# Optimization experiments

Hardware: AMD Instinct MI355X
Metric: run time of the kernel (lower is better)

The kernel has to match this reference:

```python
import jax, jax.numpy as jnp
import numpy as np

N = 100000   # nodes per graph (protein == ligand node count, forced by cat dim=1)
E = 3200000  # edges per graph (avg degree 32)
F = 128      # input feature dim
A = 10       # action dim


def _fanin_uniform(key, shape, fanin=None):
    fanin = fanin or shape[0]
    v = 1.0 / np.sqrt(fanin)
    return jax.random.uniform(key, shape, jnp.float32, -v, v)


def setup_inputs() -> dict:
    key = jax.random.key(0)
    ks = jax.random.split(key, 24)
    inp = {
        "protein_x": jax.random.normal(ks[0], (N, F), jnp.float32),
        "protein_edges": jax.random.randint(ks[1], (2, E), 0, N, jnp.int32),
        "ligand_x": jax.random.normal(ks[2], (N, F), jnp.float32),
        "ligand_edges": jax.random.randint(ks[3], (2, E), 0, N, jnp.int32),
        "action": jax.random.normal(ks[4], (N, A), jnp.float32),
        # protein GraphConv layers
        "wp1s": _fanin_uniform(ks[5], (F, 16)),
        "wp1n": _fanin_uniform(ks[6], (F, 16)),
        "bp1": jnp.zeros((16,), jnp.float32),
        "wp2s": _fanin_uniform(ks[7], (16, 50)),
        "wp2n": _fanin_uniform(ks[8], (16, 50)),
        "bp2": jnp.zeros((50,), jnp.float32),
        # ligand GraphConv layers
        "wl1s": _fanin_uniform(ks[9], (F, 16)),
        "wl1n": _fanin_uniform(ks[10], (F, 16)),
        "bl1": jnp.zeros((16,), jnp.float32),
        "wl2s": _fanin_uniform(ks[11], (16, 50)),
        "wl2n": _fanin_uniform(ks[12], (16, 50)),
        "bl2": jnp.zeros((50,), jnp.float32),
        # MLP head
        "w_in": _fanin_uniform(ks[13], (100, 60)),
        "b_in": jnp.zeros((60,), jnp.float32),
        "w_hid": _fanin_uniform(ks[14], (60 + A, 10)),
        "b_hid": jnp.zeros((10,), jnp.float32),
        "w_out": jax.random.uniform(ks[15], (10, 1), jnp.float32, -0.003, 0.003),
        "b_out": jnp.zeros((1,), jnp.float32),
    }
    return inp


def graph_conv(x, edge_index, w_self, w_nbr, b):
    # PyG GraphConv: x_i' = x_i @ W_self + (sum_{j->i} x_j) @ W_nbr + b
    src, dst = edge_index[0], edge_index[1]
    agg = jax.ops.segment_sum(x[src], dst, num_segments=x.shape[0])  # [N, Fin]
    return x @ w_self + agg @ w_nbr + b


def reference(protein_x, protein_edges, ligand_x, ligand_edges, action,
              wp1s, wp1n, bp1, wp2s, wp2n, bp2,
              wl1s, wl1n, bl1, wl2s, wl2n, bl2,
              w_in, b_in, w_hid, b_hid, w_out, b_out):
    # protein branch (dropout is identity in eval mode)
    p = jax.nn.relu(graph_conv(protein_x, protein_edges, wp1s, wp1n, bp1))
    p = graph_conv(p, protein_edges, wp2s, wp2n, bp2)            # [N, 50]
    # ligand branch
    l = jax.nn.relu(graph_conv(ligand_x, ligand_edges, wl1s, wl1n, bl1))
    l = graph_conv(l, ligand_edges, wl2s, wl2n, bl2)             # [N, 50]
    molecule = jnp.concatenate([p, l], axis=1)                   # [N, 100]
    finger_print = jax.nn.relu(molecule @ w_in + b_in)           # [N, 60]
    policy = jnp.concatenate([finger_print, action], axis=1) @ w_hid + b_hid
    policy = jax.nn.relu(policy) @ w_out + b_out                 # [N, 1]
    return policy
```

## Files before the change

### kernel.cpp

```cpp
#include <hip/hip_runtime.h>
#include <hip/hip_bf16.h>
#include <stdint.h>


#define F_IN 128
#define NBMAX 512
#define BIN_CH 16
#define BIN_EDGES (256 * BIN_CH)
#define FINE_CAP 12288

#define OW1P  0
#define OB1P  4096
#define OW1L  4112
#define OB1L  8208
#define OC1P  8224
#define OC2P  9184
#define OC1L  10144
#define OC2L  11104
#define OBIN  12064
#define OWHID 12124
#define OBHID 12824
#define OWOUT 12834
#define OBOUT 12844
#define WBUF_FLOATS 16384

__device__ __forceinline__ float bf2f(unsigned short u) {
    union { unsigned int i; float f; } v; v.i = ((unsigned int)u) << 16; return v.f;
}
__device__ __forceinline__ float bflo(unsigned int u) {
    union { unsigned int i; float f; } v; v.i = u << 16; return v.f;
}
__device__ __forceinline__ float bfhi(unsigned int u) {
    union { unsigned int i; float f; } v; v.i = u & 0xffff0000u; return v.f;
}
__device__ __forceinline__ unsigned short f2bf(float f) {
    union { float f; unsigned int i; } v; v.f = f;
    unsigned int u = v.i;
    unsigned int r = (u + 0x7fffu + ((u >> 16) & 1u)) >> 16;
    return (unsigned short)r;
}
__device__ __forceinline__ unsigned pack2bf(float a, float b) {
    return (unsigned)f2bf(a) | ((unsigned)f2bf(b) << 16);
}
__device__ __forceinline__ float ldf(const void* p, int isf32, size_t i) {
    return isf32 ? ((const float*)p)[i] : bf2f(((const unsigned short*)p)[i]);
}


struct PW {
    const void *wp1s, *wp1n, *bp1, *wl1s, *wl1n, *bl1;
    const void *wp2s, *wp2n, *bp2, *wl2s, *wl2n, *bl2;
    const void *w_in, *b_in, *w_hid, *b_hid, *w_out, *b_out;
};

__global__ __launch_bounds__(256) void k_prepw(
    PW P, const unsigned short* __restrict__ px, float* __restrict__ wb,
    int* __restrict__ flag, int* __restrict__ zp, int zn)
{
    __shared__ int cnt_s;
    if (threadIdx.x == 0) cnt_s = 0;
    __syncthreads();
    int bad = 0;
    for (int i = threadIdx.x; i < 4096; i += 256) {
        unsigned e = (px[i] >> 7) & 0xFFu;
        if (e >= 140u) bad++;
    }
    atomicAdd(&cnt_s, bad);
    __syncthreads();
    const int isf32 = (cnt_s > 4096 / 16) ? 1 : 0;
    if (threadIdx.x == 0 && blockIdx.x == 0) *flag = isf32;

    int t = blockIdx.x * 256 + threadIdx.x;
    int stride = gridDim.x * 256;
    for (int i = t; i < zn; i += stride) zp[i] = 0;

    for (int i = t; i < 4096; i += stride) {
        int k = i >> 5, j = i & 31;
        wb[OW1P + i] = (j < 16) ? ldf(P.wp1s, isf32, k * 16 + j)
                                : ldf(P.wp1n, isf32, k * 16 + (j - 16));
        wb[OW1L + i] = (j < 16) ? ldf(P.wl1s, isf32, k * 16 + j)
                                : ldf(P.wl1n, isf32, k * 16 + (j - 16));
    }
    for (int i = t; i < 16; i += stride) {
        wb[OB1P + i] = ldf(P.bp1, isf32, i);
        wb[OB1L + i] = ldf(P.bl1, isf32, i);
    }
    for (int i = t; i < 960; i += stride) {
        int k = i / 60, j = i % 60;
        float s1 = 0.f, s2 = 0.f;
        for (int r = 0; r < 50; ++r) {
            float wi = ldf(P.w_in, isf32, r * 60 + j);
            s1 += ldf(P.wp2s, isf32, k * 50 + r) * wi;
            s2 += ldf(P.wp2n, isf32, k * 50 + r) * wi;
        }
        wb[OC1P + i] = s1; wb[OC2P + i] = s2;
    }
    for (int i = t; i < 960; i += stride) {
        int k = i / 60, j = i % 60;
        float s1 = 0.f, s2 = 0.f;
        for (int r = 0; r < 50; ++r) {
            float wi = ldf(P.w_in, isf32, (50 + r) * 60 + j);
            s1 += ldf(P.wl2s, isf32, k * 50 + r) * wi;
            s2 += ldf(P.wl2n, isf32, k * 50 + r) * wi;
        }
        wb[OC1L + i] = s1; wb[OC2L + i] = s2;
    }
    for (int i = t; i < 60; i += stride) {
        float s = ldf(P.b_in, isf32, i);
        for (int r = 0; r < 50; ++r) {
            s += ldf(P.bp2, isf32, r) * ldf(P.w_in, isf32, r * 60 + i);
            s += ldf(P.bl2, isf32, r) * ldf(P.w_in, isf32, (50 + r) * 60 + i);
        }
        wb[OBIN + i] = s;
    }
    for (int i = t; i < 700; i += stride) wb[OWHID + i] = ldf(P.w_hid, isf32, i);
    for (int i = t; i < 10; i += stride) {
        wb[OBHID + i] = ldf(P.b_hid, isf32, i);
        wb[OWOUT + i] = ldf(P.w_out, isf32, i);
    }
    if (t == 0) wb[OBOUT] = ldf(P.b_out, isf32, 0);
}


__global__ __launch_bounds__(256) void k_bucket_hist(
    const int* __restrict__ ed0, const int* __restrict__ ed1,
    int* __restrict__ cnt, int nE)
{
    const int* ed = blockIdx.y ? ed1 : ed0;
    int* c = cnt + blockIdx.y * NBMAX;
    __shared__ int h[NBMAX];
    for (int i = threadIdx.x; i < NBMAX; i += 256) h[i] = 0;
    __syncthreads();
    int gid = blockIdx.x * 256 + threadIdx.x;
    int stride = gridDim.x * 256;
    int nE4 = nE >> 2;
    const int4* ed4 = (const int4*)ed;
    for (int i = gid; i < nE4; i += stride) {
        int4 v = ed4[i];
        atomicAdd(&h[v.x >> 8], 1);
        atomicAdd(&h[v.y >> 8], 1);
        atomicAdd(&h[v.z >> 8], 1);
        atomicAdd(&h[v.w >> 8], 1);
    }
    for (int e = (nE4 << 2) + gid; e < nE; e += stride)
        atomicAdd(&h[ed[e] >> 8], 1);
    __syncthreads();
    for (int i = threadIdx.x; i < NBMAX; i += 256)
        if (h[i]) atomicAdd(&c[i], h[i]);
}

__global__ __launch_bounds__(512) void k_bucket_scan(
    const int* __restrict__ cnt, int* __restrict__ base,
    int* __restrict__ cursor, int nb)
{
    const int* c = cnt + blockIdx.x * NBMAX;
    int* ba = base + blockIdx.x * 528;
    int* cu = cursor + blockIdx.x * NBMAX;
    __shared__ int sh[512];
    int t = threadIdx.x;
    int v = (t < nb) ? c[t] : 0;
    sh[t] = v;
    __syncthreads();
    for (int off = 1; off < 512; off <<= 1) {
        int x = (t >= off) ? sh[t - off] : 0;
        __syncthreads();
        sh[t] += x;
        __syncthreads();
    }
    int excl = sh[t] - v;
    if (t < nb) { ba[t] = excl; cu[t] = excl; }
    if (t == nb - 1) ba[nb] = excl + v;
}

__global__ __launch_bounds__(256) void k_bucket_bin(
    const int* __restrict__ es0, const int* __restrict__ ed0,
    const int* __restrict__ es1, const int* __restrict__ ed1,
    int* __restrict__ cursor, unsigned* __restrict__ pairs, int nE)
{
    const int* es = blockIdx.y ? es1 : es0;
    const int* ed = blockIdx.y ? ed1 : ed0;
    int* cur = cursor + blockIdx.y * NBMAX;
    unsigned* pr = pairs + (size_t)blockIdx.y * nE;

    __shared__ int h[NBMAX];
    __shared__ int lcur[NBMAX];
    __shared__ int sh[256];
    __shared__ unsigned stage[BIN_EDGES];
    __shared__ unsigned short stageB[BIN_EDGES];

    for (int i = threadIdx.x; i < NBMAX; i += 256) h[i] = 0;
    __syncthreads();
    int e0 = blockIdx.x * BIN_EDGES;
    int eb = e0 + threadIdx.x * BIN_CH;
    int s[BIN_CH], d[BIN_CH];
    if (eb + BIN_CH <= nE) {
#pragma unroll
        for (int k4 = 0; k4 < BIN_CH / 4; ++k4) {
            int4 sv = *(const int4*)(es + eb + k4 * 4);
            int4 dv = *(const int4*)(ed + eb + k4 * 4);
            s[k4 * 4 + 0] = sv.x; d[k4 * 4 + 0] = dv.x;
            s[k4 * 4 + 1] = sv.y; d[k4 * 4 + 1] = dv.y;
            s[k4 * 4 + 2] = sv.z; d[k4 * 4 + 2] = dv.z;
            s[k4 * 4 + 3] = sv.w; d[k4 * 4 + 3] = dv.w;
        }
#pragma unroll
        for (int k = 0; k < BIN_CH; ++k)
            atomicAdd(&h[d[k] >> 8], 1);
    } else {
#pragma unroll
        for (int k = 0; k < BIN_CH; ++k) {
            int e = eb + k;
            if (e < nE) {
                s[k] = es[e]; d[k] = ed[e];
                atomicAdd(&h[d[k] >> 8], 1);
            } else d[k] = -1;
        }
    }
    __syncthreads();
    {
        int t = threadIdx.x;
        int a = h[2 * t], b2 = h[2 * t + 1];
        sh[t] = a + b2;
        __syncthreads();
        for (int off = 1; off < 256; off <<= 1) {
            int x = (t >= off) ? sh[t - off] : 0;
            __syncthreads();
            sh[t] += x;
            __syncthreads();
        }
        int excl = sh[t] - (a + b2);
        lcur[2 * t] = excl;
        lcur[2 * t + 1] = excl + a;
    }
    __syncthreads();
    for (int b = threadIdx.x; b < NBMAX; b += 256) {
        int c = h[b];
        if (c) {
            int g = atomicAdd(&cur[b], c);
            h[b] = g - lcur[b];
        }
    }
    __syncthreads();
    if (eb + BIN_CH <= nE) {
#pragma unroll
        for (int k = 0; k < BIN_CH; ++k) {
            int b = d[k] >> 8;
            int pos = atomicAdd(&lcur[b], 1);
            stage[pos] = ((unsigned)(d[k] & 255) << 24) | (unsigned)s[k];
            stageB[pos] = (unsigned short)b;
        }
    } else {
#pragma unroll
        for (int k = 0; k < BIN_CH; ++k) {
            if (d[k] >= 0) {
                int b = d[k] >> 8;
                int pos = atomicAdd(&lcur[b], 1);
                stage[pos] = ((unsigned)(d[k] & 255) << 24) | (unsigned)s[k];
                stageB[pos] = (unsigned short)b;
            }
        }
    }
    __syncthreads();
    int total = nE - e0; if (total > BIN_EDGES) total = BIN_EDGES;
    for (int i = threadIdx.x; i < total; i += 256)
        pr[h[stageB[i]] + i] = stage[i];
}

__global__ __launch_bounds__(512) void k_bucket_fine(
    const unsigned* __restrict__ pairs, const int* __restrict__ base,
    int* __restrict__ row0, int* __restrict__ srcs0,
    int* __restrict__ row1, int* __restrict__ srcs1,
    int n, int nE, int nb)
{
    const unsigned* pr = pairs + (size_t)blockIdx.y * nE;
    const int* ba = base + blockIdx.y * 528;
    int* row = blockIdx.y ? row1 : row0;
    int* srcs = blockIdx.y ? srcs1 : srcs0;
    __shared__ int cnt[256], cur[256];
    __shared__ int stage[FINE_CAP];
    int b = blockIdx.x;
    int t = threadIdx.x;
    int s0 = ba[b], s1 = ba[b + 1];
    int m = s1 - s0;
    if (t < 256) cnt[t] = 0;
    __syncthreads();
    for (int i = s0 + t; i < s1; i += 512)
        atomicAdd(&cnt[pr[i] >> 24], 1);
    __syncthreads();
    int c = (t < 256) ? cnt[t] : 0;
    if (t < 256) cur[t] = c;
    __syncthreads();
    for (int off = 1; off < 256; off <<= 1) {
        int x = (t < 256 && t >= off) ? cur[t - off] : 0;
        __syncthreads();
        if (t < 256) cur[t] += x;
        __syncthreads();
    }
    int excl = (t < 256) ? (cur[t] - c) : 0;
    __syncthreads();
    int node = (b << 8) + t;
    if (t < 256 && node < n) row[node] = s0 + excl;
    if (b == nb - 1 && t == 0) row[n] = nE;
    if (m <= FINE_CAP) {
        if (t < 256) cur[t] = excl;
        __syncthreads();
        for (int i = s0 + t; i < s1; i += 512) {
            unsigned p = pr[i];
            int slot = atomicAdd(&cur[p >> 24], 1);
            stage[slot] = (int)(p & 0xFFFFFFu);
        }
        __syncthreads();
        for (int i = t; i < m; i += 512)
            srcs[s0 + i] = stage[i];
    } else {
        if (t < 256) cur[t] = s0 + excl;
        __syncthreads();
        for (int i = s0 + t; i < s1; i += 512) {
            unsigned p = pr[i];
            int slot = atomicAdd(&cur[p >> 24], 1);
            srcs[slot] = (int)(p & 0xFFFFFFu);
        }
    }
}


struct TArgs2 {
    const void* __restrict__ x;
    const float* __restrict__ w;
    const float* __restrict__ b;
    float* __restrict__ acc;
    void* __restrict__ nbr;
};

__global__ __launch_bounds__(512) void k_transform1(
    TArgs2 a0, TArgs2 a1, int n, const int* __restrict__ flag)
{
    TArgs2 A = blockIdx.y ? a1 : a0;
    const int isf32 = *flag;
    __shared__ float xs[64 * 128];
    const int t = threadIdx.x;
    const int tile0 = blockIdx.x * 64;

    if (isf32) {
        const float4* xg = (const float4*)A.x;
        float4* xl = (float4*)xs;
#pragma unroll
        for (int i = 0; i < 4; ++i) {
            int flat = i * 512 + t;
            int row = flat >> 5, ck = flat & 31;
            if (tile0 + row < n)
                xl[row * 32 + (ck ^ (row & 7))] =
                    xg[((size_t)(tile0 + row)) * 32 + ck];
        }
    } else {
        const uint4* xg = (const uint4*)A.x;
        float4* xl = (float4*)xs;
#pragma unroll
        for (int i = 0; i < 2; ++i) {
            int flat = i * 512 + t;
            int row = flat >> 4, ck = flat & 15;
            if (tile0 + row < n) {
                uint4 q = xg[((size_t)(tile0 + row)) * 16 + ck];
                float4 lo = make_float4(bflo(q.x), bfhi(q.x), bflo(q.y), bfhi(q.y));
                float4 hi = make_float4(bflo(q.z), bfhi(q.z), bflo(q.w), bfhi(q.w));
                xl[row * 32 + ((2 * ck) ^ (row & 7))] = lo;
                xl[row * 32 + ((2 * ck + 1) ^ (row & 7))] = hi;
            }
        }
    }
    __syncthreads();

    const int jq = __builtin_amdgcn_readfirstlane(t >> 6);
    const int r = t & 63;
    const int node = tile0 + r;
    if (node >= n) return;
    const float* __restrict__ Wb = A.w + 4 * jq;
    const int sw = r & 7;

    float acc[4];
    if (jq < 4) {
#pragma unroll
        for (int j = 0; j < 4; ++j) acc[j] = A.b[4 * jq + j];
    } else {
#pragma unroll
        for (int j = 0; j < 4; ++j) acc[j] = 0.f;
    }

    const float4* xl = (const float4*)xs + r * 32;
    for (int kb = 0; kb < 4; ++kb) {
        float4 xq[8];
#pragma unroll
        for (int u = 0; u < 8; ++u)
            xq[u] = xl[(kb * 8 + u) ^ sw];
#pragma unroll
        for (int u = 0; u < 8; ++u) {
            int kk = kb * 8 + u;
            float xv[4] = {xq[u].x, xq[u].y, xq[u].z, xq[u].w};
#pragma unroll
            for (int h = 0; h < 4; ++h) {
                const float* __restrict__ w0 = Wb + (kk * 4 + h) * 32;
#pragma unroll
                for (int j = 0; j < 4; ++j) acc[j] += xv[h] * w0[j];
            }
        }
    }

    if (jq < 4) {
        float4* a4 = (float4*)(A.acc + (size_t)node * 16);
        a4[jq] = make_float4(acc[0], acc[1], acc[2], acc[3]);
    } else {
        unsigned short* nrow = (unsigned short*)A.nbr + ((size_t)node << 4)
                               + ((jq - 4) << 2);
        *(uint2*)nrow = make_uint2(pack2bf(acc[0], acc[1]),
                                   pack2bf(acc[2], acc[3]));
    }
}

struct GArgs { const int *row, *srcs; const void* val; float* out; void* rout; };

__global__ __launch_bounds__(256) void k_gather16(
    GArgs g0, GArgs g1, int n, int selfmode)
{
    GArgs G = (blockIdx.x & 1) ? g1 : g0;
    int t = (blockIdx.x >> 1) * 256 + threadIdx.x;
    int node = t >> 2;
    if (node >= n) return;
    const int q = t & 3;
    const int e2 = q >> 1;
    const int c = (q & 1) << 3;
    const unsigned short* vb = (const unsigned short*)G.val;
    int rs = G.row[node], re = G.row[node + 1];
    int half = (re - rs + 1) >> 1;
    int jb = e2 ? (rs + half) : rs;
    int je = e2 ? re : (rs + half);
    float4 sa = make_float4(0.f, 0.f, 0.f, 0.f);
    float4 sb = make_float4(0.f, 0.f, 0.f, 0.f);
    int j = jb;
    for (; j + 16 <= je; j += 16) {
        int s[16];
        uint4 v[16];
#pragma unroll
        for (int u = 0; u < 16; ++u) s[u] = G.srcs[j + u];
#pragma unroll
        for (int u = 0; u < 16; ++u)
            v[u] = *(const uint4*)(vb + (((size_t)s[u]) << 4) + c);
#pragma unroll
        for (int u = 0; u < 16; ++u) {
            sa.x += bflo(v[u].x); sa.y += bfhi(v[u].x);
            sa.z += bflo(v[u].y); sa.w += bfhi(v[u].y);
            sb.x += bflo(v[u].z); sb.y += bfhi(v[u].z);
            sb.z += bflo(v[u].w); sb.w += bfhi(v[u].w);
        }
    }
    for (; j + 8 <= je; j += 8) {
        int s[8];
        uint4 v[8];
#pragma unroll
        for (int u = 0; u < 8; ++u) s[u] = G.srcs[j + u];
#pragma unroll
        for (int u = 0; u < 8; ++u)
            v[u] = *(const uint4*)(vb + (((size_t)s[u]) << 4) + c);
#pragma unroll
        for (int u = 0; u < 8; ++u) {
            sa.x += bflo(v[u].x); sa.y += bfhi(v[u].x);
            sa.z += bflo(v[u].y); sa.w += bfhi(v[u].y);
            sb.x += bflo(v[u].z); sb.y += bfhi(v[u].z);
            sb.z += bflo(v[u].w); sb.w += bfhi(v[u].w);
        }
    }
    for (; j < je; ++j) {
        uint4 v = *(const uint4*)(vb + (((size_t)G.srcs[j]) << 4) + c);
        sa.x += bflo(v.x); sa.y += bfhi(v.x);
        sa.z += bflo(v.y); sa.w += bfhi(v.y);
        sb.x += bflo(v.z); sb.y += bfhi(v.z);
        sb.z += bflo(v.w); sb.w += bfhi(v.w);
    }
    sa.x += __shfl_xor(sa.x, 2); sa.y += __shfl_xor(sa.y, 2);
    sa.z += __shfl_xor(sa.z, 2); sa.w += __shfl_xor(sa.w, 2);
    sb.x += __shfl_xor(sb.x, 2); sb.y += __shfl_xor(sb.y, 2);
    sb.z += __shfl_xor(sb.z, 2); sb.w += __shfl_xor(sb.w, 2);
    if (e2 == 0) {
        float4* o4 = (float4*)(G.out + ((size_t)node << 4) + c);
        if (selfmode) {
            float4 pa = o4[0], pb = o4[1];
            sa.x += pa.x; sa.y += pa.y; sa.z += pa.z; sa.w += pa.w;
            sb.x += pb.x; sb.y += pb.y; sb.z += pb.z; sb.w += pb.w;
        }
        o4[0] = sa; o4[1] = sb;
        if (selfmode) {
            unsigned short* orow = (unsigned short*)G.rout + ((size_t)node << 4) + c;
            *(uint4*)orow = make_uint4(
                pack2bf(fmaxf(sa.x, 0.f), fmaxf(sa.y, 0.f)),
                pack2bf(fmaxf(sa.z, 0.f), fmaxf(sa.w, 0.f)),
                pack2bf(fmaxf(sb.x, 0.f), fmaxf(sb.y, 0.f)),
                pack2bf(fmaxf(sb.z, 0.f), fmaxf(sb.w, 0.f)));
        }
    }
}

__device__ __forceinline__ void fp_acc30(float* fp, const float* __restrict__ wb,
                                         int off, int jo,
                                         const float* __restrict__ row, bool dorelu)
{
    const float4* r4 = (const float4*)row;
    for (int kk = 0; kk < 4; ++kk) {
        float4 v = r4[kk];
        float xs[4] = {v.x, v.y, v.z, v.w};
        if (dorelu) {
            xs[0] = fmaxf(xs[0], 0.f); xs[1] = fmaxf(xs[1], 0.f);
            xs[2] = fmaxf(xs[2], 0.f); xs[3] = fmaxf(xs[3], 0.f);
        }
        const float* __restrict__ wq = wb + off + kk * 240 + jo;
#pragma unroll
        for (int h = 0; h < 4; ++h) {
#pragma unroll
            for (int j = 0; j < 30; ++j) fp[j] += xs[h] * wq[h * 60 + j];
        }
    }
}

__global__ __launch_bounds__(256) void k_headf(
    const float* __restrict__ hP, const float* __restrict__ gP,
    const float* __restrict__ hL, const float* __restrict__ gL,
    const void* __restrict__ action, const float* __restrict__ wb,
    void* __restrict__ out, int n, const int* __restrict__ flag)
{
    const int isf32 = *flag;
    __shared__ float hbuf[128][10];
    int w = threadIdx.x >> 6;
    int jh = __builtin_amdgcn_readfirstlane(w & 1);
    int slot = ((w >> 1) << 6) + (threadIdx.x & 63);
    int node = blockIdx.x * 128 + slot;
    int nodec = node < n ? node : (n - 1);
    const int jo = 30 * jh;

    float fp[30];
#pragma unroll
    for (int j = 0; j < 30; ++j) fp[j] = wb[OBIN + jo + j];

    fp_acc30(fp, wb, OC1P, jo, hP + (size_t)nodec * 16, true);
    fp_acc30(fp, wb, OC2P, jo, gP + (size_t)nodec * 16, false);
    fp_acc30(fp, wb, OC1L, jo, hL + (size_t)nodec * 16, true);
    fp_acc30(fp, wb, OC2L, jo, gL + (size_t)nodec * 16, false);

    float h[10];
#pragma unroll
    for (int j = 0; j < 10; ++j) h[j] = (jh == 0) ? wb[OBHID + j] : 0.f;
#pragma unroll
    for (int k = 0; k < 30; ++k) {
        float v = fmaxf(fp[k], 0.f);
#pragma unroll
        for (int j = 0; j < 10; ++j) h[j] += v * wb[OWHID + (jo + k) * 10 + j];
    }
    if (jh) {
#pragma unroll
        for (int j = 0; j < 10; ++j) hbuf[slot][j] = h[j];
    }
    __syncthreads();
    if (jh == 0) {
#pragma unroll
        for (int j = 0; j < 10; ++j) h[j] += hbuf[slot][j];
#pragma unroll
        for (int k = 0; k < 10; ++k) {
            float v = ldf(action, isf32, (size_t)nodec * 10 + k);
#pragma unroll
            for (int j = 0; j < 10; ++j) h[j] += v * wb[OWHID + (60 + k) * 10 + j];
        }
        float o = wb[OBOUT];
#pragma unroll
        for (int j = 0; j < 10; ++j) o += fmaxf(h[j], 0.f) * wb[OWOUT + j];
        if (node < n) {
            if (isf32) ((float*)out)[node] = o;
            else       ((unsigned short*)out)[node] = f2bf(o);
        }
    }
}

extern "C" void kernel_launch(void* const* d_in, const int* in_sizes, int n_in,
                              void* d_out, int out_size, void* d_ws, size_t ws_size,
                              hipStream_t stream)
{
    const void* px   = d_in[0];
    const int*  pe   = (const int*)d_in[1];
    const void* lx   = d_in[2];
    const int*  le   = (const int*)d_in[3];
    const void* act  = d_in[4];

    const int N = in_sizes[0] / F_IN;
    const int E = in_sizes[1] / 2;
    const int NB = (N + 255) >> 8;

    int* flag    = (int*)d_ws;
    int* cnt     = flag + 64;
    int* base    = cnt + 2 * NBMAX;
    int* cursorB = base + 2 * 528;
    float* wbuf  = (float*)(flag + 3200);
    int* rowP    = flag + 3200 + WBUF_FLOATS;
    int* srcsP   = rowP + (N + 64);
    int* rowL    = srcsP + E;
    int* srcsL   = rowL + (N + 64);
    float* dense = (float*)(srcsL + E);
    unsigned* pairs = (unsigned*)dense;

    float* accP = dense;
    float* accL = accP + (size_t)N * 16;
    float* aggP = accL + (size_t)N * 16;
    float* aggL = aggP + (size_t)N * 16;
    void*  n1P  = (void*)(aggL + (size_t)N * 16);
    void*  n1L  = (void*)((float*)n1P + (size_t)N * 8);
    void*  n2P  = (void*)((float*)n1L + (size_t)N * 8);
    void*  n2L  = (void*)((float*)n2P + (size_t)N * 8);

    const int nb64 = (N + 63) / 64;
    const int nb128 = (N + 127) / 128;
    const int gb4 = (N * 4 + 255) / 256;
    const int bb = (E + BIN_EDGES - 1) / BIN_EDGES;

    PW P{d_in[5], d_in[6], d_in[7], d_in[11], d_in[12], d_in[13],
         d_in[8], d_in[9], d_in[10], d_in[14], d_in[15], d_in[16],
         d_in[17], d_in[18], d_in[19], d_in[20], d_in[21], d_in[22]};
    k_prepw<<<64, 256, 0, stream>>>(P, (const unsigned short*)px, wbuf,
                                    flag, cnt, 2 * NBMAX);

    k_bucket_hist<<<dim3(256, 2), 256, 0, stream>>>(pe + E, le + E, cnt, E);
    k_bucket_scan<<<2, 512, 0, stream>>>(cnt, base, cursorB, NB);
    k_bucket_bin<<<dim3(bb, 2), 256, 0, stream>>>(pe, pe + E, le, le + E,
                                                  cursorB, pairs, E);
    k_bucket_fine<<<dim3(NB, 2), 512, 0, stream>>>(pairs, base, rowP, srcsP,
                                                   rowL, srcsL, N, E, NB);

    TArgs2 tP{px, wbuf + OW1P, wbuf + OB1P, accP, n1P};
    TArgs2 tL{lx, wbuf + OW1L, wbuf + OB1L, accL, n1L};
    k_transform1<<<dim3(nb64, 2), 512, 0, stream>>>(tP, tL, N, flag);

    GArgs g1P{rowP, srcsP, n1P, accP, n2P}, g1L{rowL, srcsL, n1L, accL, n2L};
    k_gather16<<<gb4 * 2, 256, 0, stream>>>(g1P, g1L, N, 1);

    GArgs g2P{rowP, srcsP, n2P, aggP, nullptr}, g2L{rowL, srcsL, n2L, aggL, nullptr};
    k_gather16<<<gb4 * 2, 256, 0, stream>>>(g2P, g2L, N, 0);

    k_headf<<<nb128, 256, 0, stream>>>(accP, aggP, accL, aggL, act, wbuf,
                                       d_out, N, flag);
}
```

Baseline: 434.6 us.

## Replace CSR build and per-node gather with bucket-based LDS atomic aggregation

Drops the fine bucketing kernel that built the CSR row/srcs arrays. The two gather passes now read the coarse-binned (dst_local, src) pairs directly. Each block owns one 256-node bucket and accumulates neighbour features with shared-memory float atomics into a 16x256 tile. This removes one kernel launch and the CSR write/read traffic, at the cost of many LDS atomics per edge (16 per edge) and non-deterministic summation order.

```diff
diff --git a/kernel.cpp b/kernel.cpp
--- a/kernel.cpp
+++ b/kernel.cpp
@@ -7,7 +7,6 @@
 #define NBMAX 512
 #define BIN_CH 16
 #define BIN_EDGES (256 * BIN_CH)
-#define FINE_CAP 12288
 
 #define OW1P  0
 #define OB1P  4096
@@ -266,63 +265,6 @@
         pr[h[stageB[i]] + i] = stage[i];
 }
 
-__global__ __launch_bounds__(512) void k_bucket_fine(
-    const unsigned* __restrict__ pairs, const int* __restrict__ base,
-    int* __restrict__ row0, int* __restrict__ srcs0,
-    int* __restrict__ row1, int* __restrict__ srcs1,
-    int n, int nE, int nb)
-{
-    const unsigned* pr = pairs + (size_t)blockIdx.y * nE;
-    const int* ba = base + blockIdx.y * 528;
-    int* row = blockIdx.y ? row1 : row0;
-    int* srcs = blockIdx.y ? srcs1 : srcs0;
-    __shared__ int cnt[256], cur[256];
-    __shared__ int stage[FINE_CAP];
-    int b = blockIdx.x;
-    int t = threadIdx.x;
-    int s0 = ba[b], s1 = ba[b + 1];
-    int m = s1 - s0;
-    if (t < 256) cnt[t] = 0;
-    __syncthreads();
-    for (int i = s0 + t; i < s1; i += 512)
-        atomicAdd(&cnt[pr[i] >> 24], 1);
-    __syncthreads();
-    int c = (t < 256) ? cnt[t] : 0;
-    if (t < 256) cur[t] = c;
-    __syncthreads();
-    for (int off = 1; off < 256; off <<= 1) {
-        int x = (t < 256 && t >= off) ? cur[t - off] : 0;
-        __syncthreads();
-        if (t < 256) cur[t] += x;
-        __syncthreads();
-    }
-    int excl = (t < 256) ? (cur[t] - c) : 0;
-    __syncthreads();
-    int node = (b << 8) + t;
-    if (t < 256 && node < n) row[node] = s0 + excl;
-    if (b == nb - 1 && t == 0) row[n] = nE;
-    if (m <= FINE_CAP) {
-        if (t < 256) cur[t] = excl;
-        __syncthreads();
-        for (int i = s0 + t; i < s1; i += 512) {
-            unsigned p = pr[i];
-            int slot = atomicAdd(&cur[p >> 24], 1);
-            stage[slot] = (int)(p & 0xFFFFFFu);
-        }
-        __syncthreads();
-        for (int i = t; i < m; i += 512)
-            srcs[s0 + i] = stage[i];
-    } else {
-        if (t < 256) cur[t] = s0 + excl;
-        __syncthreads();
-        for (int i = s0 + t; i < s1; i += 512) {
-            unsigned p = pr[i];
-            int slot = atomicAdd(&cur[p >> 24], 1);
-            srcs[slot] = (int)(p & 0xFFFFFFu);
-        }
-    }
-}
-
 
 struct TArgs2 {
     const void* __restrict__ x;
@@ -416,84 +358,87 @@
     }
 }
 
-struct GArgs { const int *row, *srcs; const void* val; float* out; void* rout; };
-
-__global__ __launch_bounds__(256) void k_gather16(
-    GArgs g0, GArgs g1, int n, int selfmode)
-{
-    GArgs G = (blockIdx.x & 1) ? g1 : g0;
-    int t = (blockIdx.x >> 1) * 256 + threadIdx.x;
-    int node = t >> 2;
-    if (node >= n) return;
-    const int q = t & 3;
-    const int e2 = q >> 1;
-    const int c = (q & 1) << 3;
+
+struct GB { const void* val; const float* self; float* out; void* rout; };
+
+__global__ __launch_bounds__(512) void k_gather_bkt(
+    const unsigned* __restrict__ pairs, const int* __restrict__ base,
+    GB g0, GB g1, int n, int nE, int selfmode)
+{
+    const int g = blockIdx.x & 1;
+    const int b = blockIdx.x >> 1;
+    GB G = g ? g1 : g0;
+    const unsigned* pr = pairs + (size_t)g * nE;
+    const int* ba = base + g * 528;
     const unsigned short* vb = (const unsigned short*)G.val;
-    int rs = G.row[node], re = G.row[node + 1];
-    int half = (re - rs + 1) >> 1;
-    int jb = e2 ? (rs + half) : rs;
-    int je = e2 ? re : (rs + half);
-    float4 sa = make_float4(0.f, 0.f, 0.f, 0.f);
-    float4 sb = make_float4(0.f, 0.f, 0.f, 0.f);
-    int j = jb;
-    for (; j + 16 <= je; j += 16) {
-        int s[16];
-        uint4 v[16];
-#pragma unroll
-        for (int u = 0; u < 16; ++u) s[u] = G.srcs[j + u];
-#pragma unroll
-        for (int u = 0; u < 16; ++u)
-            v[u] = *(const uint4*)(vb + (((size_t)s[u]) << 4) + c);
-#pragma unroll
-        for (int u = 0; u < 16; ++u) {
-            sa.x += bflo(v[u].x); sa.y += bfhi(v[u].x);
-            sa.z += bflo(v[u].y); sa.w += bfhi(v[u].y);
-            sb.x += bflo(v[u].z); sb.y += bfhi(v[u].z);
-            sb.z += bflo(v[u].w); sb.w += bfhi(v[u].w);
-        }
-    }
-    for (; j + 8 <= je; j += 8) {
-        int s[8];
+    __shared__ float acc[16][256];
+    const int t = threadIdx.x;
+    for (int i = t; i < 4096; i += 512) ((float*)acc)[i] = 0.f;
+    __syncthreads();
+    const int s0 = ba[b], s1 = ba[b + 1];
+    int i = s0 + t;
+    for (; i + 3 * 512 < s1; i += 4 * 512) {
+        unsigned p[4];
         uint4 v[8];
 #pragma unroll
-        for (int u = 0; u < 8; ++u) s[u] = G.srcs[j + u];
-#pragma unroll
-        for (int u = 0; u < 8; ++u)
-            v[u] = *(const uint4*)(vb + (((size_t)s[u]) << 4) + c);
-#pragma unroll
-        for (int u = 0; u < 8; ++u) {
-            sa.x += bflo(v[u].x); sa.y += bfhi(v[u].x);
-            sa.z += bflo(v[u].y); sa.w += bfhi(v[u].y);
-            sb.x += bflo(v[u].z); sb.y += bfhi(v[u].z);
-            sb.z += bflo(v[u].w); sb.w += bfhi(v[u].w);
-        }
-    }
-    for (; j < je; ++j) {
-        uint4 v = *(const uint4*)(vb + (((size_t)G.srcs[j]) << 4) + c);
-        sa.x += bflo(v.x); sa.y += bfhi(v.x);
-        sa.z += bflo(v.y); sa.w += bfhi(v.y);
-        sb.x += bflo(v.z); sb.y += bfhi(v.z);
-        sb.z += bflo(v.w); sb.w += bfhi(v.w);
-    }
-    sa.x += __shfl_xor(sa.x, 2); sa.y += __shfl_xor(sa.y, 2);
-    sa.z += __shfl_xor(sa.z, 2); sa.w += __shfl_xor(sa.w, 2);
-    sb.x += __shfl_xor(sb.x, 2); sb.y += __shfl_xor(sb.y, 2);
-    sb.z += __shfl_xor(sb.z, 2); sb.w += __shfl_xor(sb.w, 2);
-    if (e2 == 0) {
-        float4* o4 = (float4*)(G.out + ((size_t)node << 4) + c);
+        for (int u = 0; u < 4; ++u) p[u] = pr[i + u * 512];
+#pragma unroll
+        for (int u = 0; u < 4; ++u) {
+            const uint4* vr = (const uint4*)(vb + (((size_t)(p[u] & 0xFFFFFFu)) << 4));
+            v[2 * u] = vr[0]; v[2 * u + 1] = vr[1];
+        }
+#pragma unroll
+        for (int u = 0; u < 4; ++u) {
+            int dl = p[u] >> 24;
+            uint4 a = v[2 * u], c4 = v[2 * u + 1];
+            atomicAdd(&acc[0][dl],  bflo(a.x));  atomicAdd(&acc[1][dl],  bfhi(a.x));
+            atomicAdd(&acc[2][dl],  bflo(a.y));  atomicAdd(&acc[3][dl],  bfhi(a.y));
+            atomicAdd(&acc[4][dl],  bflo(a.z));  atomicAdd(&acc[5][dl],  bfhi(a.z));
+            atomicAdd(&acc[6][dl],  bflo(a.w));  atomicAdd(&acc[7][dl],  bfhi(a.w));
+            atomicAdd(&acc[8][dl],  bflo(c4.x)); atomicAdd(&acc[9][dl],  bfhi(c4.x));
+            atomicAdd(&acc[10][dl], bflo(c4.y)); atomicAdd(&acc[11][dl], bfhi(c4.y));
+            atomicAdd(&acc[12][dl], bflo(c4.z)); atomicAdd(&acc[13][dl], bfhi(c4.z));
+            atomicAdd(&acc[14][dl], bflo(c4.w)); atomicAdd(&acc[15][dl], bfhi(c4.w));
+        }
+    }
+    for (; i < s1; i += 512) {
+        unsigned p = pr[i];
+        const uint4* vr = (const uint4*)(vb + (((size_t)(p & 0xFFFFFFu)) << 4));
+        uint4 a = vr[0], c4 = vr[1];
+        int dl = p >> 24;
+        atomicAdd(&acc[0][dl],  bflo(a.x));  atomicAdd(&acc[1][dl],  bfhi(a.x));
+        atomicAdd(&acc[2][dl],  bflo(a.y));  atomicAdd(&acc[3][dl],  bfhi(a.y));
+        atomicAdd(&acc[4][dl],  bflo(a.z));  atomicAdd(&acc[5][dl],  bfhi(a.z));
+        atomicAdd(&acc[6][dl],  bflo(a.w));  atomicAdd(&acc[7][dl],  bfhi(a.w));
+        atomicAdd(&acc[8][dl],  bflo(c4.x)); atomicAdd(&acc[9][dl],  bfhi(c4.x));
+        atomicAdd(&acc[10][dl], bflo(c4.y)); atomicAdd(&acc[11][dl], bfhi(c4.y));
+        atomicAdd(&acc[12][dl], bflo(c4.z)); atomicAdd(&acc[13][dl], bfhi(c4.z));
+        atomicAdd(&acc[14][dl], bflo(c4.w)); atomicAdd(&acc[15][dl], bfhi(c4.w));
+    }
+    __syncthreads();
+    const int dl = t >> 1;
+    const int node = (b << 8) + dl;
+    const int ch = (t & 1) << 3;
+    if (node < n) {
+        float o[8];
+#pragma unroll
+        for (int j = 0; j < 8; ++j) o[j] = acc[ch + j][dl];
         if (selfmode) {
-            float4 pa = o4[0], pb = o4[1];
-            sa.x += pa.x; sa.y += pa.y; sa.z += pa.z; sa.w += pa.w;
-            sb.x += pb.x; sb.y += pb.y; sb.z += pb.z; sb.w += pb.w;
-        }
-        o4[0] = sa; o4[1] = sb;
+            const float4* s4 = (const float4*)(G.self + ((size_t)node << 4) + ch);
+            float4 x0 = s4[0], x1 = s4[1];
+            o[0] += x0.x; o[1] += x0.y; o[2] += x0.z; o[3] += x0.w;
+            o[4] += x1.x; o[5] += x1.y; o[6] += x1.z; o[7] += x1.w;
+        }
+        float4* o4 = (float4*)(G.out + ((size_t)node << 4) + ch);
+        o4[0] = make_float4(o[0], o[1], o[2], o[3]);
+        o4[1] = make_float4(o[4], o[5], o[6], o[7]);
         if (selfmode) {
-            unsigned short* orow = (unsigned short*)G.rout + ((size_t)node << 4) + c;
+            unsigned short* orow = (unsigned short*)G.rout + ((size_t)node << 4) + ch;
             *(uint4*)orow = make_uint4(
-                pack2bf(fmaxf(sa.x, 0.f), fmaxf(sa.y, 0.f)),
-                pack2bf(fmaxf(sa.z, 0.f), fmaxf(sa.w, 0.f)),
-                pack2bf(fmaxf(sb.x, 0.f), fmaxf(sb.y, 0.f)),
-                pack2bf(fmaxf(sb.z, 0.f), fmaxf(sb.w, 0.f)));
+                pack2bf(fmaxf(o[0], 0.f), fmaxf(o[1], 0.f)),
+                pack2bf(fmaxf(o[2], 0.f), fmaxf(o[3], 0.f)),
+                pack2bf(fmaxf(o[4], 0.f), fmaxf(o[5], 0.f)),
+                pack2bf(fmaxf(o[6], 0.f), fmaxf(o[7], 0.f)));
         }
     }
 }
@@ -595,12 +540,8 @@
     int* base    = cnt + 2 * NBMAX;
     int* cursorB = base + 2 * 528;
     float* wbuf  = (float*)(flag + 3200);
-    int* rowP    = flag + 3200 + WBUF_FLOATS;
-    int* srcsP   = rowP + (N + 64);
-    int* rowL    = srcsP + E;
-    int* srcsL   = rowL + (N + 64);
-    float* dense = (float*)(srcsL + E);
-    unsigned* pairs = (unsigned*)dense;
+    unsigned* pairs = (unsigned*)(wbuf + WBUF_FLOATS);
+    float* dense = (float*)(pairs + 2 * (size_t)E);
 
     float* accP = dense;
     float* accL = accP + (size_t)N * 16;
@@ -613,7 +554,6 @@
 
     const int nb64 = (N + 63) / 64;
     const int nb128 = (N + 127) / 128;
-    const int gb4 = (N * 4 + 255) / 256;
     const int bb = (E + BIN_EDGES - 1) / BIN_EDGES;
 
     PW P{d_in[5], d_in[6], d_in[7], d_in[11], d_in[12], d_in[13],
@@ -626,18 +566,16 @@
     k_bucket_scan<<<2, 512, 0, stream>>>(cnt, base, cursorB, NB);
     k_bucket_bin<<<dim3(bb, 2), 256, 0, stream>>>(pe, pe + E, le, le + E,
                                                   cursorB, pairs, E);
-    k_bucket_fine<<<dim3(NB, 2), 512, 0, stream>>>(pairs, base, rowP, srcsP,
-                                                   rowL, srcsL, N, E, NB);
 
     TArgs2 tP{px, wbuf + OW1P, wbuf + OB1P, accP, n1P};
     TArgs2 tL{lx, wbuf + OW1L, wbuf + OB1L, accL, n1L};
     k_transform1<<<dim3(nb64, 2), 512, 0, stream>>>(tP, tL, N, flag);
 
-    GArgs g1P{rowP, srcsP, n1P, accP, n2P}, g1L{rowL, srcsL, n1L, accL, n2L};
-    k_gather16<<<gb4 * 2, 256, 0, stream>>>(g1P, g1L, N, 1);
-
-    GArgs g2P{rowP, srcsP, n2P, aggP, nullptr}, g2L{rowL, srcsL, n2L, aggL, nullptr};
-    k_gather16<<<gb4 * 2, 256, 0, stream>>>(g2P, g2L, N, 0);
+    GB b1P{n1P, accP, accP, n2P}, b1L{n1L, accL, accL, n2L};
+    k_gather_bkt<<<NB * 2, 512, 0, stream>>>(pairs, base, b1P, b1L, N, E, 1);
+
+    GB b2P{n2P, nullptr, aggP, nullptr}, b2L{n2L, nullptr, aggL, nullptr};
+    k_gather_bkt<<<NB * 2, 512, 0, stream>>>(pairs, base, b2P, b2L, N, E, 0);
 
     k_headf<<<nb128, 256, 0, stream>>>(accP, aggP, accL, aggL, act, wbuf,
                                        d_out, N, flag);
```

Result: slower. 1.662 ms (+282.4%).
